# Kernel optimization log

Measured on AMD Instinct MI355X. Metric: run time of the kernel, lower is better.

## Reference

```python
import jax, jax.numpy as jnp
import numpy as np
from jax.scipy.special import gammaln, xlogy

DIM = 1536
HEADS = 8
DK = 64
DV = 64
BS = 128
N = 1536
NRPF = 192  # num_rel_pos_features, divisible by 6
B = 2


def _positional_embed(n, feat):
    # [2n-1, feat] relative positional basis (exponential, central-mask, gamma),
    # each duplicated with sign(d) asymmetric variant.
    f = feat // 6
    d = jnp.arange(-n + 1, n, dtype=jnp.float32)
    ad = jnp.abs(d)[:, None]  # [2n-1, 1]
    # exponential: log-spaced half lives
    half_life = 2.0 ** jnp.linspace(3.0, float(np.log2(n)), f)
    e_exp = jnp.exp(-float(np.log(2.0)) / half_life[None, :] * ad)
    # central mask: 1 if |d| < 2^i - 1
    widths = 2.0 ** jnp.arange(1, f + 1, dtype=jnp.float32) - 1.0
    e_cm = (widths[None, :] > ad).astype(jnp.float32)
    # gamma pdf, linearly spaced means
    std = n / (2.0 * f)
    mean = jnp.linspace(n / f, float(n), f)[None, :]
    conc = (mean / std) ** 2
    rate = mean / (std ** 2)
    log_unnorm = xlogy(conc - 1.0, ad) - rate * ad
    log_norm = gammaln(conc) - conc * jnp.log(rate)
    probs = jnp.exp(log_unnorm - log_norm) + 1e-8
    e_g = probs / jnp.max(probs, axis=-1, keepdims=True)
    emb = jnp.concatenate([e_exp, e_cm, e_g], axis=-1)  # [2n-1, 3f]
    return jnp.concatenate([emb, jnp.sign(d)[:, None] * emb], axis=-1)  # [2n-1, 6f]


def _relative_shift(t):
    # [B, H, N, 2N-1] -> [B, H, N, N] (Transformer-XL shift)
    b, h, t1, t2 = t.shape
    t = jnp.concatenate([jnp.zeros_like(t[..., :1]), t], axis=-1)  # [.., t2+1]
    t = t.reshape(b, h, t2 + 1, t1)[:, :, 1:, :].reshape(b, h, t1, t2)
    return t[..., :t1]


def setup_inputs() -> dict:
    key = jax.random.key(0)
    ks = jax.random.split(key, 10)
    x = jax.random.normal(ks[0], (B, N, DIM), dtype=jnp.float32)
    Wq = jax.random.normal(ks[1], (DIM, HEADS * DK), dtype=jnp.float32) * 0.02
    Wk = jax.random.normal(ks[2], (DIM, HEADS * DK), dtype=jnp.float32) * 0.02
    Wv = jax.random.normal(ks[3], (DIM, HEADS * DV), dtype=jnp.float32) * 0.02
    Wrel = jax.random.normal(ks[4], (NRPF, HEADS * DK), dtype=jnp.float32) * 0.02
    rel_content_bias = jax.random.normal(ks[5], (1, HEADS, 1, DK), dtype=jnp.float32)
    rel_pos_bias = jax.random.normal(ks[6], (1, HEADS, 1, DK), dtype=jnp.float32)
    # to_out is zero-init in the original; use small random so the output/grads are non-trivial
    Wo = jax.random.normal(ks[7], (HEADS * DV, DIM), dtype=jnp.float32) * 0.02
    bo = jnp.zeros((DIM,), dtype=jnp.float32)
    pos_embed = _positional_embed(N, NRPF)  # [2N-1, NRPF]
    # BigBird block-local window mask: blocks bi attend to blocks bi-1..bi+1
    bi = np.arange(N) // BS
    local_mask = jnp.asarray(np.abs(bi[:, None] - bi[None, :]) <= 1)  # [N, N] bool
    # a few global tokens per batch
    is_global = jnp.zeros((B, N), dtype=bool).at[:, :4].set(True)
    return {"x": x, "Wq": Wq, "Wk": Wk, "Wv": Wv, "Wrel": Wrel,
            "rel_content_bias": rel_content_bias, "rel_pos_bias": rel_pos_bias,
            "Wo": Wo, "bo": bo, "pos_embed": pos_embed,
            "local_mask": local_mask, "is_global": is_global}


def reference(x, Wq, Wk, Wv, Wrel, rel_content_bias, rel_pos_bias, Wo, bo,
              pos_embed, local_mask, is_global):
    b, n, _ = x.shape
    h, dk = rel_content_bias.shape[1], rel_content_bias.shape[-1]
    dv = Wv.shape[-1] // h
    scale = dk ** -0.5
    q = (x @ Wq).reshape(b, n, h, dk).transpose(0, 2, 1, 3) * scale  # [b,h,n,dk]
    k = (x @ Wk).reshape(b, n, h, dk).transpose(0, 2, 1, 3)
    v = (x @ Wv).reshape(b, n, h, dv).transpose(0, 2, 1, 3)
    content_logits = jnp.einsum('bhid,bhjd->bhij', q + rel_content_bias, k)
    rel_k = (pos_embed @ Wrel).reshape(2 * n - 1, h, dk).transpose(1, 0, 2)  # [h,2n-1,dk]
    rel_logits = jnp.einsum('bhid,hjd->bhij', q + rel_pos_bias, rel_k)  # [b,h,n,2n-1]
    logits = content_logits + _relative_shift(rel_logits)
    attn_bool = (local_mask[None, None] | is_global[:, None, :, None]
                 | is_global[:, None, None, :])
    logits = jnp.where(attn_bool, logits.astype(jnp.float32), -jnp.inf)
    attn = jax.nn.softmax(logits, axis=-1)
    out = jnp.einsum('bhij,bhjd->bhid', attn, v.astype(jnp.float32))
    out = out.astype(x.dtype).transpose(0, 2, 1, 3).reshape(b, n, h * dv)
    return out @ Wo + bo
```

## Files before the change

### kernel.cpp

```cpp
#include <hip/hip_runtime.h>
#include <math.h>

#define NSEQ 1536
#define HD3  1536
#define RKLD 512
#define RLEN 3071
#define NB   12

typedef __attribute__((ext_vector_type(8))) short bf16x8;
typedef __attribute__((ext_vector_type(4))) float f32x4;
typedef _Float16 f16x8 __attribute__((ext_vector_type(8)));
typedef _Float16 f16x4 __attribute__((ext_vector_type(4)));

__device__ __forceinline__ unsigned short f2bf(float f) {
    union { float f; unsigned u; } v; v.f = f;
    unsigned r = v.u + 0x7fffu + ((v.u >> 16) & 1u);
    return (unsigned short)(r >> 16);
}
__device__ __forceinline__ float bf2f(unsigned short s) {
    union { unsigned u; float f; } v; v.u = ((unsigned)s) << 16;
    return v.f;
}
__device__ __forceinline__ void cp16(const void* g, void* l) {
    __builtin_amdgcn_global_load_lds(
        (const __attribute__((address_space(1))) void*)g,
        (__attribute__((address_space(3))) void*)l, 16, 0, 0);
}

#define KSWZ(row, d) ((row) * 64 + (((((d) >> 3) ^ ((row) & 7))) << 3) + ((d) & 7))
#define PSWZ(r, j)   ((r) * 128 + (((((j) >> 3) ^ ((r) & 15))) << 3) + ((j) & 7))
#define VSTR 136

__global__ __launch_bounds__(256) void splitf16(
    const float* __restrict__ X, _Float16* __restrict__ H, int n4)
{
    int i = blockIdx.x * 256 + threadIdx.x;
    if (i >= n4) return;
    float4 v = ((const float4*)X)[i];
    union { _Float16 h[4]; ushort4 u; } c;
    c.h[0] = (_Float16)v.x; c.h[1] = (_Float16)v.y;
    c.h[2] = (_Float16)v.z; c.h[3] = (_Float16)v.w;
    ((ushort4*)H)[i] = c.u;
}

__device__ __forceinline__ void wsplit_body16(
    const float* __restrict__ W, _Float16* __restrict__ T,
    int K, int N, int n_off, int ldt, float scale, int bx, int by)
{
    __shared__ float tile[64][65];
    const int k0 = by * 64, n0 = bx * 64;
    const int t = threadIdx.x;
    const int rr = t >> 4, c4 = (t & 15) * 4;
#pragma unroll
    for (int p = 0; p < 4; ++p) {
        int r = p * 16 + rr;
        float4 v = *(const float4*)(W + (size_t)(k0 + r) * N + n0 + c4);
        tile[r][c4 + 0] = v.x; tile[r][c4 + 1] = v.y;
        tile[r][c4 + 2] = v.z; tile[r][c4 + 3] = v.w;
    }
    __syncthreads();
#pragma unroll
    for (int p = 0; p < 4; ++p) {
        int n = p * 16 + rr;
        union { _Float16 h[4]; ushort4 u; } cc;
        cc.h[0] = (_Float16)(tile[c4 + 0][n] * scale);
        cc.h[1] = (_Float16)(tile[c4 + 1][n] * scale);
        cc.h[2] = (_Float16)(tile[c4 + 2][n] * scale);
        cc.h[3] = (_Float16)(tile[c4 + 3][n] * scale);
        size_t o = (size_t)(n_off + n0 + n) * ldt + k0 + c4;
        *(ushort4*)(T + o) = cc.u;
    }
}

__global__ __launch_bounds__(256) void wsplit_qkv16(
    const float* __restrict__ Wq, const float* __restrict__ Wk,
    const float* __restrict__ Wv, _Float16* __restrict__ T)
{
    const int z = blockIdx.z;
    const float* W = (z == 0) ? Wq : (z == 1) ? Wk : Wv;
    wsplit_body16(W, T, 1536, 512, z * 512, 1536, (z == 0) ? 0.125f : 1.f,
                  blockIdx.x, blockIdx.y);
}

__global__ __launch_bounds__(256) void wsplit_t16(
    const float* __restrict__ W, _Float16* __restrict__ T,
    int K, int N, int n_off, int ldt, float scale)
{
    wsplit_body16(W, T, K, N, n_off, ldt, scale, blockIdx.x, blockIdx.y);
}

__global__ __launch_bounds__(256) void gemm_f16k(
    const _Float16* __restrict__ A,
    const _Float16* __restrict__ B,
    const float* __restrict__ bias, float* __restrict__ C,
    int M, int N, int K)
{
    __shared__ _Float16 sA[2][4096];
    __shared__ _Float16 sB[2][4096];
    const int t = threadIdx.x;
    const int wave = t >> 6, lane = t & 63;
    const int nwg = gridDim.x * gridDim.y;
    const int lin = blockIdx.y * gridDim.x + blockIdx.x;
    const int swz = (lin & 7) * (nwg >> 3) + (lin >> 3);
    const int bx = swz % gridDim.x, by = swz / gridDim.x;
    const int m0 = by * 64, n0 = bx * 64;
    const int wm = (wave >> 1) * 32, wn = (wave & 1) * 32;
    const int fr = lane & 15, quad = lane >> 4;

    f32x4 acc[2][2];
#pragma unroll
    for (int i = 0; i < 2; ++i)
#pragma unroll
        for (int j = 0; j < 2; ++j)
#pragma unroll
            for (int c = 0; c < 4; ++c) acc[i][j][c] = 0.f;

    const int nsteps = K >> 6;

#define STAGE(k0, buf)                                                        \
    {                                                                         \
        _Pragma("unroll")                                                     \
        for (int it = 0; it < 2; ++it) {                                      \
            int cidx = it * 256 + t;                                          \
            int row = cidx >> 3, slot = cidx & 7;                             \
            int gch = slot ^ (row & 7);                                       \
            size_t goA = (size_t)(m0 + row) * K + (k0) + gch * 8;             \
            size_t goB = (size_t)(n0 + row) * K + (k0) + gch * 8;             \
            cp16(A + goA, &sA[buf][it * 2048 + wave * 512]);                  \
            cp16(B + goB, &sB[buf][it * 2048 + wave * 512]);                  \
        }                                                                     \
    }

    STAGE(0, 0);
    for (int s = 0; s < nsteps; ++s) {
        const int buf = s & 1;
        __syncthreads();
        if (s + 1 < nsteps) STAGE((s + 1) * 64, buf ^ 1);

        f16x8 fa[2][2], fb[2][2];
#pragma unroll
        for (int ti = 0; ti < 2; ++ti)
#pragma unroll
            for (int kc = 0; kc < 2; ++kc) {
                fa[ti][kc] = *(const f16x8*)&sA[buf][KSWZ(wm + ti * 16 + fr,
                                                          kc * 32 + quad * 8)];
                fb[ti][kc] = *(const f16x8*)&sB[buf][KSWZ(wn + ti * 16 + fr,
                                                          kc * 32 + quad * 8)];
            }
#pragma unroll
        for (int ti = 0; ti < 2; ++ti)
#pragma unroll
            for (int tj = 0; tj < 2; ++tj)
#pragma unroll
                for (int kc = 0; kc < 2; ++kc)
                    acc[ti][tj] = __builtin_amdgcn_mfma_f32_16x16x32_f16(
                        fa[ti][kc], fb[tj][kc], acc[ti][tj], 0, 0, 0);
    }
#undef STAGE

#pragma unroll
    for (int ti = 0; ti < 2; ++ti) {
        int rowb = m0 + wm + ti * 16 + quad * 4;
#pragma unroll
        for (int tj = 0; tj < 2; ++tj) {
            int col = n0 + wn + tj * 16 + fr;
            float bb = bias ? bias[col] : 0.f;
#pragma unroll
            for (int j2 = 0; j2 < 4; ++j2)
                C[(size_t)(rowb + j2) * N + col] = acc[ti][tj][j2] + bb;
        }
    }
}

__global__ __launch_bounds__(256) void gemm_f32(
    const float* __restrict__ A, const float* __restrict__ B,
    const float* __restrict__ bias, float* __restrict__ C,
    int M, int N, int K, float alpha)
{
    __shared__ float As_[16][68];
    __shared__ float Bs_[16][68];
    const int t = threadIdx.x;
    const int m0 = blockIdx.y * 64;
    const int n0 = blockIdx.x * 64;
    const int tm = t >> 4, tn = t & 15;
    float acc[4][4];
#pragma unroll
    for (int i = 0; i < 4; ++i)
#pragma unroll
        for (int j = 0; j < 4; ++j) acc[i][j] = 0.f;

    for (int k0 = 0; k0 < K; k0 += 16) {
        {
            int row = t >> 2;
            int kk  = (t & 3) * 4;
            int gm  = m0 + row;
            float4 av = make_float4(0.f, 0.f, 0.f, 0.f);
            if (gm < M) av = *(const float4*)(A + (size_t)gm * K + k0 + kk);
            As_[kk + 0][row] = av.x; As_[kk + 1][row] = av.y;
            As_[kk + 2][row] = av.z; As_[kk + 3][row] = av.w;
        }
        {
            int kk = t >> 4;
            int nn = (t & 15) * 4;
            float4 bv = *(const float4*)(B + (size_t)(k0 + kk) * N + n0 + nn);
            *(float4*)&Bs_[kk][nn] = bv;
        }
        __syncthreads();
#pragma unroll
        for (int kk = 0; kk < 16; ++kk) {
            float a[4], bb[4];
            *(float4*)&a[0]  = *(const float4*)&As_[kk][tm * 4];
            *(float4*)&bb[0] = *(const float4*)&Bs_[kk][tn * 4];
#pragma unroll
            for (int i = 0; i < 4; ++i)
#pragma unroll
                for (int j = 0; j < 4; ++j)
                    acc[i][j] = fmaf(a[i], bb[j], acc[i][j]);
        }
        __syncthreads();
    }
#pragma unroll
    for (int i = 0; i < 4; ++i) {
        int gm = m0 + tm * 4 + i;
        if (gm < M) {
            float* crow = C + (size_t)gm * N + n0 + tn * 4;
#pragma unroll
            for (int j = 0; j < 4; ++j) {
                float vv = acc[i][j] * alpha;
                if (bias) vv += bias[n0 + tn * 4 + j];
                crow[j] = vv;
            }
        }
    }
}

__global__ __launch_bounds__(256) void drk_kernel(
    const float* __restrict__ rkk, const float* __restrict__ cb,
    const float* __restrict__ rb, float* __restrict__ drk)
{
    int idx = blockIdx.x * 256 + threadIdx.x;
    if (idx >= 8 * RLEN) return;
    int jj = idx >> 3, h = idx & 7;
    const float* rrow = rkk + (size_t)jj * RKLD + h * 64;
    float s0 = 0, s1 = 0, s2 = 0, s3 = 0;
#pragma unroll
    for (int d4 = 0; d4 < 16; ++d4) {
        float4 rv = *(const float4*)(rrow + d4 * 4);
        float dx = rb[h * 64 + d4 * 4 + 0] - cb[h * 64 + d4 * 4 + 0];
        float dy = rb[h * 64 + d4 * 4 + 1] - cb[h * 64 + d4 * 4 + 1];
        float dz = rb[h * 64 + d4 * 4 + 2] - cb[h * 64 + d4 * 4 + 2];
        float dw = rb[h * 64 + d4 * 4 + 3] - cb[h * 64 + d4 * 4 + 3];
        s0 = fmaf(dx, rv.x, s0); s1 = fmaf(dy, rv.y, s1);
        s2 = fmaf(dz, rv.z, s2); s3 = fmaf(dw, rv.w, s3);
    }
    drk[h * RLEN + jj] = (s0 + s1) + (s2 + s3);
}

__global__ __launch_bounds__(256) void relb_mfma(
    const float* __restrict__ qkv, const float* __restrict__ rkk,
    const float* __restrict__ rb, _Float16* __restrict__ relbT)
{
    __shared__ _Float16 sR[8192];
    const int ct = blockIdx.x, bi = blockIdx.y, bh = blockIdx.z;
    const int b = bh >> 3, h = bh & 7;
    const int i0 = bi * 128;
    const int c0 = (bi == 0) ? 0 : (bi - 1) * 128;
    const int jjbase = c0 - i0 - 127 + (NSEQ - 1) + ct * 128;
    const int t = threadIdx.x;
    const int wave = t >> 6, lane = t & 63;
    const int fr = lane & 15, quad = lane >> 4;

#pragma unroll
    for (int it = 0; it < 8; ++it) {
        int lin = it * 256 + t;
        int row = lin >> 4, d4 = (lin & 15) * 4;
        const float* rp = rkk + (size_t)(jjbase + row) * RKLD + h * 64 + d4;
        float4 v = *(const float4*)rp;
        union { _Float16 h[4]; ushort4 u; } cc;
        cc.h[0] = (_Float16)v.x; cc.h[1] = (_Float16)v.y;
        cc.h[2] = (_Float16)v.z; cc.h[3] = (_Float16)v.w;
        *(ushort4*)&sR[KSWZ(row, d4)] = cc.u;
    }
    f16x8 qf[2][2];
    {
        const float* Qg = qkv + ((size_t)(b * NSEQ + i0)) * HD3 + h * 64;
#pragma unroll
        for (int ti = 0; ti < 2; ++ti)
#pragma unroll
            for (int kc = 0; kc < 2; ++kc) {
                int m = wave * 32 + ti * 16 + fr;
                int k8 = kc * 32 + quad * 8;
                const float* qp = Qg + (size_t)m * HD3 + k8;
                const float* cp = rb + h * 64 + k8;
                float4 qa = *(const float4*)qp,  qb = *(const float4*)(qp + 4);
                float4 ca = *(const float4*)cp,  c2 = *(const float4*)(cp + 4);
                _Float16 hx[8] = {
                    (_Float16)(qa.x + ca.x), (_Float16)(qa.y + ca.y),
                    (_Float16)(qa.z + ca.z), (_Float16)(qa.w + ca.w),
                    (_Float16)(qb.x + c2.x), (_Float16)(qb.y + c2.y),
                    (_Float16)(qb.z + c2.z), (_Float16)(qb.w + c2.w)};
                qf[ti][kc] = *(f16x8*)hx;
            }
    }
    __syncthreads();

    f32x4 sacc[2][8];
#pragma unroll
    for (int i = 0; i < 2; ++i)
#pragma unroll
        for (int j = 0; j < 8; ++j)
#pragma unroll
            for (int c = 0; c < 4; ++c) sacc[i][j][c] = 0.f;

#pragma unroll
    for (int kc = 0; kc < 2; ++kc) {
        f16x8 bv[8];
#pragma unroll
        for (int tj = 0; tj < 8; ++tj)
            bv[tj] = *(const f16x8*)&sR[KSWZ(tj * 16 + fr, kc * 32 + quad * 8)];
#pragma unroll
        for (int ti = 0; ti < 2; ++ti)
#pragma unroll
            for (int tj = 0; tj < 8; ++tj)
                sacc[ti][tj] = __builtin_amdgcn_mfma_f32_16x16x32_f16(
                    qf[ti][kc], bv[tj], sacc[ti][tj], 0, 0, 0);
    }

    size_t bb_ = ((size_t)bh * NB + bi) * 512;
#pragma unroll
    for (int ti = 0; ti < 2; ++ti) {
        int mr = wave * 32 + ti * 16 + quad * 4;
#pragma unroll
        for (int tj = 0; tj < 8; ++tj) {
            int ccg = ct * 128 + tj * 16 + fr;
#pragma unroll
            for (int reg = 0; reg < 4; ++reg) {
                int r = mr + reg;
                int jl = ccg - 127 + r;
                if (jl >= 0)
                    relbT[(bb_ + jl) * 128 + r] = (_Float16)sacc[ti][tj][reg];
            }
        }
    }
}

__global__ __launch_bounds__(256) void attn_mfma(
    const float* __restrict__ qkv, const _Float16* __restrict__ relbT,
    const float* __restrict__ cb, float* __restrict__ O_part,
    float* __restrict__ l_part)
{
    __shared__ unsigned short sKP[16384];
    __shared__ unsigned short sVt[64 * VSTR];
    const int ct = blockIdx.x, bi = blockIdx.y, bh = blockIdx.z;
    const int b = bh >> 3, h = bh & 7;
    const int i0 = bi * 128;
    const int c0 = (bi == 0) ? 0 : (bi - 1) * 128;
    const int c1 = (bi == NB - 1) ? NSEQ : (bi + 2) * 128;
    const int ctile = c0 + ct * 128;
    const int t = threadIdx.x;
    const int wave = t >> 6, lane = t & 63;
    const int fr = lane & 15, quad = lane >> 4;

    float* Op = O_part + (((size_t)ct * 16 + bh) * NSEQ + i0) * 64;
    float* lp = l_part + ((size_t)ct * 16 + bh) * NSEQ + i0;

    if (ctile >= c1) {
        for (int k2 = t; k2 < 8192; k2 += 256) Op[k2] = 0.f;
        if (t < 128) lp[t] = 0.f;
        return;
    }

    {
        const float* Kg = qkv + ((size_t)(b * NSEQ + ctile)) * HD3 + 512 + h * 64;
#pragma unroll
        for (int it = 0; it < 8; ++it) {
            int lin = it * 256 + t;
            int row = lin >> 4, d4 = (lin & 15) * 4;
            float4 v = *(const float4*)(Kg + (size_t)row * HD3 + d4);
            union { _Float16 h[4]; ushort4 u; } cc;
            cc.h[0] = (_Float16)v.x; cc.h[1] = (_Float16)v.y;
            cc.h[2] = (_Float16)v.z; cc.h[3] = (_Float16)v.w;
            *(ushort4*)&sKP[KSWZ(row, d4)] = cc.u;
        }
    }
    {
        const float* Vg = qkv + ((size_t)(b * NSEQ + ctile)) * HD3 + 1024 + h * 64;
#pragma unroll
        for (int it = 0; it < 2; ++it) {
            int lin = it * 256 + t;
            int r4 = (lin >> 4) * 4, d4 = (lin & 15) * 4;
            float4 v0 = *(const float4*)(Vg + (size_t)(r4 + 0) * HD3 + d4);
            float4 v1 = *(const float4*)(Vg + (size_t)(r4 + 1) * HD3 + d4);
            float4 v2 = *(const float4*)(Vg + (size_t)(r4 + 2) * HD3 + d4);
            float4 v3 = *(const float4*)(Vg + (size_t)(r4 + 3) * HD3 + d4);
            const float* p0 = (const float*)&v0;
            const float* p1 = (const float*)&v1;
            const float* p2 = (const float*)&v2;
            const float* p3 = (const float*)&v3;
#pragma unroll
            for (int dd = 0; dd < 4; ++dd) {
                ushort4 hh;
                hh.x = f2bf(p0[dd]); hh.y = f2bf(p1[dd]);
                hh.z = f2bf(p2[dd]); hh.w = f2bf(p3[dd]);
                *(ushort4*)&sVt[(d4 + dd) * VSTR + r4] = hh;
            }
        }
    }
    f16x8 qf[2][2];
    {
        const float* Qg = qkv + ((size_t)(b * NSEQ + i0)) * HD3 + h * 64;
#pragma unroll
        for (int ti = 0; ti < 2; ++ti)
#pragma unroll
            for (int kc = 0; kc < 2; ++kc) {
                int m = wave * 32 + ti * 16 + fr;
                int k8 = kc * 32 + quad * 8;
                const float* qp = Qg + (size_t)m * HD3 + k8;
                const float* cp = cb + h * 64 + k8;
                float4 qa = *(const float4*)qp,  qb = *(const float4*)(qp + 4);
                float4 ca = *(const float4*)cp,  c2 = *(const float4*)(cp + 4);
                _Float16 hx[8] = {
                    (_Float16)(qa.x + ca.x), (_Float16)(qa.y + ca.y),
                    (_Float16)(qa.z + ca.z), (_Float16)(qa.w + ca.w),
                    (_Float16)(qb.x + c2.x), (_Float16)(qb.y + c2.y),
                    (_Float16)(qb.z + c2.z), (_Float16)(qb.w + c2.w)};
                qf[ti][kc] = *(f16x8*)hx;
            }
    }
    __syncthreads();

    f32x4 sacc[2][8];
#pragma unroll
    for (int i = 0; i < 2; ++i)
#pragma unroll
        for (int j = 0; j < 8; ++j)
#pragma unroll
            for (int c = 0; c < 4; ++c) sacc[i][j][c] = 0.f;

#pragma unroll
    for (int kc = 0; kc < 2; ++kc) {
        f16x8 bv[8];
#pragma unroll
        for (int tj = 0; tj < 8; ++tj)
            bv[tj] = *(const f16x8*)&sKP[KSWZ(tj * 16 + fr, kc * 32 + quad * 8)];
#pragma unroll
        for (int ti = 0; ti < 2; ++ti)
#pragma unroll
            for (int tj = 0; tj < 8; ++tj)
                sacc[ti][tj] = __builtin_amdgcn_mfma_f32_16x16x32_f16(
                    qf[ti][kc], bv[tj], sacc[ti][tj], 0, 0, 0);
    }
    __syncthreads();

    const _Float16* relbase = relbT + (((size_t)bh * NB + bi) * 512 + ct * 128) * 128;
    float lsum[2][4] = {{0.f, 0.f, 0.f, 0.f}, {0.f, 0.f, 0.f, 0.f}};
#pragma unroll
    for (int ti = 0; ti < 2; ++ti) {
        int mr = wave * 32 + ti * 16 + quad * 4;
#pragma unroll
        for (int tj = 0; tj < 8; ++tj) {
            int j = tj * 16 + fr;
            f16x4 rl = *(const f16x4*)&relbase[(size_t)j * 128 + mr];
#pragma unroll
            for (int reg = 0; reg < 4; ++reg) {
                int r = mr + reg;
                float p = __expf(sacc[ti][tj][reg] + (float)rl[reg]);
                unsigned short pb = f2bf(p);
                lsum[ti][reg] += bf2f(pb);
                sKP[PSWZ(r, j)] = pb;
            }
        }
    }
#pragma unroll
    for (int m2 = 1; m2 < 16; m2 <<= 1)
#pragma unroll
        for (int ti = 0; ti < 2; ++ti)
#pragma unroll
            for (int reg = 0; reg < 4; ++reg)
                lsum[ti][reg] += __shfl_xor(lsum[ti][reg], m2, 64);
    if (fr == 0) {
#pragma unroll
        for (int ti = 0; ti < 2; ++ti) {
            int mr = wave * 32 + ti * 16 + quad * 4;
#pragma unroll
            for (int reg = 0; reg < 4; ++reg)
                lp[mr + reg] = lsum[ti][reg];
        }
    }

    f32x4 oacc[4][2];
#pragma unroll
    for (int i = 0; i < 4; ++i)
#pragma unroll
        for (int j = 0; j < 2; ++j)
#pragma unroll
            for (int c = 0; c < 4; ++c) oacc[i][j][c] = 0.f;

#pragma unroll
    for (int kc = 0; kc < 4; ++kc) {
        bf16x8 pbv[2];
#pragma unroll
        for (int rt2 = 0; rt2 < 2; ++rt2) {
            int r = (wave * 2 + rt2) * 16 + fr;
            pbv[rt2] = *(const bf16x8*)&sKP[PSWZ(r, kc * 32 + quad * 8)];
        }
#pragma unroll
        for (int dt = 0; dt < 4; ++dt) {
            bf16x8 av = *(const bf16x8*)&sVt[(dt * 16 + fr) * VSTR + kc * 32 + quad * 8];
#pragma unroll
            for (int rt2 = 0; rt2 < 2; ++rt2)
                oacc[dt][rt2] = __builtin_amdgcn_mfma_f32_16x16x32_bf16(
                    av, pbv[rt2], oacc[dt][rt2], 0, 0, 0);
        }
    }
#pragma unroll
    for (int dt = 0; dt < 4; ++dt)
#pragma unroll
        for (int rt2 = 0; rt2 < 2; ++rt2) {
            int r = (wave * 2 + rt2) * 16 + fr;
            int d = dt * 16 + quad * 4;
            float4 ov = make_float4(oacc[dt][rt2][0], oacc[dt][rt2][1],
                                    oacc[dt][rt2][2], oacc[dt][rt2][3]);
            *(float4*)(Op + (size_t)r * 64 + d) = ov;
        }
}

__global__ __launch_bounds__(128) void attn_gcols(
    const float* __restrict__ qkv, const float* __restrict__ rkk,
    const float* __restrict__ drk, const float* __restrict__ cb,
    float* __restrict__ O_part, float* __restrict__ l_part)
{
    const int bi = blockIdx.x + 2, bh = blockIdx.y;
    const int b = bh >> 3, h = bh & 7;
    const int i = bi * 128 + threadIdx.x;
    float qc[64];
    {
        const float* qrow = qkv + (size_t)(b * NSEQ + i) * HD3 + h * 64;
#pragma unroll
        for (int d4 = 0; d4 < 16; ++d4) {
            float4 qv = *(const float4*)(qrow + d4 * 4);
            float4 cv = *(const float4*)(cb + h * 64 + d4 * 4);
            qc[4 * d4 + 0] = qv.x + cv.x;
            qc[4 * d4 + 1] = qv.y + cv.y;
            qc[4 * d4 + 2] = qv.z + cv.z;
            qc[4 * d4 + 3] = qv.w + cv.w;
        }
    }
    float O[64];
#pragma unroll
    for (int d = 0; d < 64; ++d) O[d] = 0.f;
    float l = 0.f;
    for (int j = 0; j < 4; ++j) {
        const float* krow = qkv + ((size_t)(b * NSEQ + j)) * HD3 + 512 + h * 64;
        int jj = j - i + (NSEQ - 1);
        const float* rrow = rkk + (size_t)jj * RKLD + h * 64;
        float s0 = 0, s1 = 0, s2 = 0, s3 = 0;
#pragma unroll
        for (int d4 = 0; d4 < 16; ++d4) {
            float4 kv = *(const float4*)(krow + d4 * 4);
            float4 rv = *(const float4*)(rrow + d4 * 4);
            s0 = fmaf(qc[4 * d4 + 0], kv.x + rv.x, s0);
            s1 = fmaf(qc[4 * d4 + 1], kv.y + rv.y, s1);
            s2 = fmaf(qc[4 * d4 + 2], kv.z + rv.z, s2);
            s3 = fmaf(qc[4 * d4 + 3], kv.w + rv.w, s3);
        }
        float p = __expf((s0 + s1) + (s2 + s3) + drk[h * RLEN + jj]);
        l += p;
        const float* vrow = krow + 512;
#pragma unroll
        for (int d4 = 0; d4 < 16; ++d4) {
            float4 vf = *(const float4*)(vrow + d4 * 4);
            O[4 * d4 + 0] = fmaf(p, vf.x, O[4 * d4 + 0]);
            O[4 * d4 + 1] = fmaf(p, vf.y, O[4 * d4 + 1]);
            O[4 * d4 + 2] = fmaf(p, vf.z, O[4 * d4 + 2]);
            O[4 * d4 + 3] = fmaf(p, vf.w, O[4 * d4 + 3]);
        }
    }
    float* Op = O_part + ((size_t)bh * NSEQ + i) * 64;
#pragma unroll
    for (int d4 = 0; d4 < 16; ++d4) {
        float4 cur = *(float4*)(Op + d4 * 4);
        cur.x += O[4 * d4 + 0]; cur.y += O[4 * d4 + 1];
        cur.z += O[4 * d4 + 2]; cur.w += O[4 * d4 + 3];
        *(float4*)(Op + d4 * 4) = cur;
    }
    l_part[(size_t)bh * NSEQ + i] += l;
}

__global__ __launch_bounds__(256) void grows_part(
    const float* __restrict__ qkv, const float* __restrict__ rkk,
    const float* __restrict__ drk, const float* __restrict__ cb,
    float* __restrict__ g_O, float* __restrict__ g_l)
{
    __shared__ float qc_s[64];
    __shared__ float p_s[128];
    __shared__ float obuf[4][64];
    __shared__ float lred[2];
    const int chunk = blockIdx.x;
    const int bhi = blockIdx.y;
    const int i = bhi & 3, h = (bhi >> 2) & 7, b = bhi >> 5;
    const int t = threadIdx.x;
    const int c0 = chunk * 128;
    if (t < 64)
        qc_s[t] = qkv[(size_t)(b * NSEQ + i) * HD3 + h * 64 + t] + cb[h * 64 + t];
    __syncthreads();
    if (t < 128) {
        int j = c0 + t;
        const float* krow = qkv + (size_t)(b * NSEQ + j) * HD3 + 512 + h * 64;
        int jj = j - i + (NSEQ - 1);
        const float* rrow = rkk + (size_t)jj * RKLD + h * 64;
        float s0 = 0, s1 = 0, s2 = 0, s3 = 0;
#pragma unroll
        for (int d4 = 0; d4 < 16; ++d4) {
            float4 kv = *(const float4*)(krow + d4 * 4);
            float4 rv = *(const float4*)(rrow + d4 * 4);
            float4 qv = *(const float4*)(&qc_s[d4 * 4]);
            s0 = fmaf(qv.x, kv.x + rv.x, s0);
            s1 = fmaf(qv.y, kv.y + rv.y, s1);
            s2 = fmaf(qv.z, kv.z + rv.z, s2);
            s3 = fmaf(qv.w, kv.w + rv.w, s3);
        }
        float p = __expf((s0 + s1) + (s2 + s3) + drk[h * RLEN + jj]);
        p_s[t] = p;
        float ls = p;
#pragma unroll
        for (int off = 32; off > 0; off >>= 1)
            ls += __shfl_down(ls, off, 64);
        if ((t & 63) == 0) lred[t >> 6] = ls;
    }
    __syncthreads();
    {
        const int d = t & 63, g = t >> 6;
        float a0 = 0, a1 = 0;
        const float* vbase = qkv + (size_t)(b * NSEQ + c0 + g * 32) * HD3 + 1024 + h * 64 + d;
#pragma unroll
        for (int j2 = 0; j2 < 32; j2 += 2) {
            a0 = fmaf(p_s[g * 32 + j2],     vbase[(size_t)j2 * HD3],       a0);
            a1 = fmaf(p_s[g * 32 + j2 + 1], vbase[(size_t)(j2 + 1) * HD3], a1);
        }
        obuf[g][d] = a0 + a1;
    }
    __syncthreads();
    if (t < 64) {
        float o = (obuf[0][t] + obuf[1][t]) + (obuf[2][t] + obuf[3][t]);
        g_O[((size_t)chunk * 64 + bhi) * 64 + t] = o;
        if (t == 0) g_l[chunk * 64 + bhi] = lred[0] + lred[1];
    }
}

__global__ __launch_bounds__(256) void norm_merge(
    const float* __restrict__ O_part, const float* __restrict__ l_part,
    const float* __restrict__ g_O, const float* __restrict__ g_l,
    _Float16* __restrict__ aoh)
{
    const int bh = blockIdx.y, b = bh >> 3, h = bh & 7;
    const int i = blockIdx.x * 16 + (threadIdx.x >> 4);
    const int d4 = threadIdx.x & 15;
    float ox = 0, oy = 0, oz = 0, ow = 0, l = 0;
    if (i < 4) {
        const int bhi = bh * 4 + i;
#pragma unroll
        for (int c = 0; c < 12; ++c) {
            const float* gp = g_O + ((size_t)c * 64 + bhi) * 64 + d4 * 4;
            ox += gp[0]; oy += gp[1]; oz += gp[2]; ow += gp[3];
            l += g_l[c * 64 + bhi];
        }
    } else {
#pragma unroll
        for (int s = 0; s < 3; ++s) {
            const float* Opp = O_part + (((size_t)s * 16 + bh) * NSEQ + i) * 64 + d4 * 4;
            float4 p = *(const float4*)Opp;
            ox += p.x; oy += p.y; oz += p.z; ow += p.w;
            l += l_part[((size_t)s * 16 + bh) * NSEQ + i];
        }
    }
    float inv = 1.f / l;
    union { _Float16 h[4]; ushort4 u; } cc;
    cc.h[0] = (_Float16)(ox * inv); cc.h[1] = (_Float16)(oy * inv);
    cc.h[2] = (_Float16)(oz * inv); cc.h[3] = (_Float16)(ow * inv);
    size_t o = ((size_t)(b * NSEQ + i)) * 512 + h * 64 + d4 * 4;
    *(ushort4*)(aoh + o) = cc.u;
}

extern "C" void kernel_launch(void* const* d_in, const int* in_sizes, int n_in,
                              void* d_out, int out_size, void* d_ws, size_t ws_size,
                              hipStream_t stream)
{
    const float* x    = (const float*)d_in[0];
    const float* Wq   = (const float*)d_in[1];
    const float* Wk   = (const float*)d_in[2];
    const float* Wv   = (const float*)d_in[3];
    const float* Wrel = (const float*)d_in[4];
    const float* cb   = (const float*)d_in[5];
    const float* rb   = (const float*)d_in[6];
    const float* Wo   = (const float*)d_in[7];
    const float* bo   = (const float*)d_in[8];
    const float* pe   = (const float*)d_in[9];
    float* out = (float*)d_out;

    float* ws = (float*)d_ws;
    float* qkv   = ws;
    float* rkbuf = ws + 4718592;
    float* drk   = ws + 6291456;
    _Float16* aoh = (_Float16*)(ws + 6316032);
    _Float16* woh = (_Float16*)(ws + 7888896);
    float* R = ws + 8675328;
    _Float16* relbT = (_Float16*)R;
    _Float16* xh  = (_Float16*)R;
    _Float16* wqh = (_Float16*)(R + 4718592);
    float* g_O = R + 6291456;
    float* g_l = R + 6340608;
    float* O_part = ws + 15753216;
    float* l_part = ws + 20471808;

    dim3 blk(256);
    splitf16<<<4608, blk, 0, stream>>>(x, xh, 1179648);
    wsplit_qkv16<<<dim3(8, 24, 3), blk, 0, stream>>>(Wq, Wk, Wv, wqh);
    wsplit_t16<<<dim3(24, 8), blk, 0, stream>>>(Wo, woh, 512, 1536, 0, 512, 1.f);
    gemm_f16k<<<dim3(24, 48), blk, 0, stream>>>(xh, wqh, nullptr, qkv,
                                                3072, 1536, 1536);
    gemm_f32<<<dim3(8, 48), blk, 0, stream>>>(pe, Wrel, nullptr, rkbuf, 3071, 512, 192, 1.f);
    drk_kernel<<<96, blk, 0, stream>>>(rkbuf, cb, rb, drk);
    relb_mfma<<<dim3(4, 12, 16), blk, 0, stream>>>(qkv, rkbuf, rb, relbT);
    attn_mfma<<<dim3(3, 12, 16), blk, 0, stream>>>(qkv, relbT, cb, O_part, l_part);
    attn_gcols<<<dim3(10, 16), dim3(128), 0, stream>>>(qkv, rkbuf, drk, cb, O_part, l_part);
    grows_part<<<dim3(12, 64), blk, 0, stream>>>(qkv, rkbuf, drk, cb, g_O, g_l);
    norm_merge<<<dim3(96, 16), blk, 0, stream>>>(O_part, l_part, g_O, g_l, aoh);
    gemm_f16k<<<dim3(24, 48), blk, 0, stream>>>(aoh, woh, bo, out,
                                                3072, 1536, 512);
}
```

Baseline: 268.2 us.

## Fuse weight splits, move rel-pos GEMM to f16 MFMA, fold global columns into attention

Three weight-transpose kernels (qkv, Wo, Wrel) are merged into one launch. The fp32 SIMT GEMM for pos_embed@Wrel is replaced by an f16 MFMA GEMM, with pos_embed converted to f16 first. The separate attn_gcols kernel is removed, and the first-4 global-column contributions are computed inside attn_mfma for the ct==0 tiles. This cuts launches and a read-modify-write pass over O_part, at the cost of f16 precision on rel-pos keys and extra work in some attention blocks. The rel-pos GEMM now runs with M=3072 over a 3071-row input, which relies on padding or workspace slack.

```diff
diff --git a/kernel.cpp b/kernel.cpp
--- a/kernel.cpp
+++ b/kernel.cpp
@@ -72,21 +72,24 @@
     }
 }
 
-__global__ __launch_bounds__(256) void wsplit_qkv16(
+__global__ __launch_bounds__(256) void wsplit_all(
     const float* __restrict__ Wq, const float* __restrict__ Wk,
-    const float* __restrict__ Wv, _Float16* __restrict__ T)
+    const float* __restrict__ Wv, const float* __restrict__ Wo,
+    const float* __restrict__ Wrel,
+    _Float16* __restrict__ Tqkv, _Float16* __restrict__ To,
+    _Float16* __restrict__ Trel)
 {
     const int z = blockIdx.z;
-    const float* W = (z == 0) ? Wq : (z == 1) ? Wk : Wv;
-    wsplit_body16(W, T, 1536, 512, z * 512, 1536, (z == 0) ? 0.125f : 1.f,
-                  blockIdx.x, blockIdx.y);
-}
-
-__global__ __launch_bounds__(256) void wsplit_t16(
-    const float* __restrict__ W, _Float16* __restrict__ T,
-    int K, int N, int n_off, int ldt, float scale)
-{
-    wsplit_body16(W, T, K, N, n_off, ldt, scale, blockIdx.x, blockIdx.y);
+    if (z < 3) {
+        const float* W = (z == 0) ? Wq : (z == 1) ? Wk : Wv;
+        wsplit_body16(W, Tqkv, 1536, 512, z * 512, 1536,
+                      (z == 0) ? 0.125f : 1.f, blockIdx.x, blockIdx.y);
+    } else if (z == 3) {
+        wsplit_body16(Wo, To, 512, 1536, 0, 512, 1.f, blockIdx.y, blockIdx.x);
+    } else {
+        if (blockIdx.y >= 3) return;
+        wsplit_body16(Wrel, Trel, 192, 512, 0, 192, 1.f, blockIdx.x, blockIdx.y);
+    }
 }
 
 __global__ __launch_bounds__(256) void gemm_f16k(
@@ -168,68 +171,6 @@
 #pragma unroll
             for (int j2 = 0; j2 < 4; ++j2)
                 C[(size_t)(rowb + j2) * N + col] = acc[ti][tj][j2] + bb;
-        }
-    }
-}
-
-__global__ __launch_bounds__(256) void gemm_f32(
-    const float* __restrict__ A, const float* __restrict__ B,
-    const float* __restrict__ bias, float* __restrict__ C,
-    int M, int N, int K, float alpha)
-{
-    __shared__ float As_[16][68];
-    __shared__ float Bs_[16][68];
-    const int t = threadIdx.x;
-    const int m0 = blockIdx.y * 64;
-    const int n0 = blockIdx.x * 64;
-    const int tm = t >> 4, tn = t & 15;
-    float acc[4][4];
-#pragma unroll
-    for (int i = 0; i < 4; ++i)
-#pragma unroll
-        for (int j = 0; j < 4; ++j) acc[i][j] = 0.f;
-
-    for (int k0 = 0; k0 < K; k0 += 16) {
-        {
-            int row = t >> 2;
-            int kk  = (t & 3) * 4;
-            int gm  = m0 + row;
-            float4 av = make_float4(0.f, 0.f, 0.f, 0.f);
-            if (gm < M) av = *(const float4*)(A + (size_t)gm * K + k0 + kk);
-            As_[kk + 0][row] = av.x; As_[kk + 1][row] = av.y;
-            As_[kk + 2][row] = av.z; As_[kk + 3][row] = av.w;
-        }
-        {
-            int kk = t >> 4;
-            int nn = (t & 15) * 4;
-            float4 bv = *(const float4*)(B + (size_t)(k0 + kk) * N + n0 + nn);
-            *(float4*)&Bs_[kk][nn] = bv;
-        }
-        __syncthreads();
-#pragma unroll
-        for (int kk = 0; kk < 16; ++kk) {
-            float a[4], bb[4];
-            *(float4*)&a[0]  = *(const float4*)&As_[kk][tm * 4];
-            *(float4*)&bb[0] = *(const float4*)&Bs_[kk][tn * 4];
-#pragma unroll
-            for (int i = 0; i < 4; ++i)
-#pragma unroll
-                for (int j = 0; j < 4; ++j)
-                    acc[i][j] = fmaf(a[i], bb[j], acc[i][j]);
-        }
-        __syncthreads();
-    }
-#pragma unroll
-    for (int i = 0; i < 4; ++i) {
-        int gm = m0 + tm * 4 + i;
-        if (gm < M) {
-            float* crow = C + (size_t)gm * N + n0 + tn * 4;
-#pragma unroll
-            for (int j = 0; j < 4; ++j) {
-                float vv = acc[i][j] * alpha;
-                if (bias) vv += bias[n0 + tn * 4 + j];
-                crow[j] = vv;
-            }
         }
     }
 }
@@ -346,11 +287,15 @@
 
 __global__ __launch_bounds__(256) void attn_mfma(
     const float* __restrict__ qkv, const _Float16* __restrict__ relbT,
+    const float* __restrict__ rkbuf, const float* __restrict__ drk,
     const float* __restrict__ cb, float* __restrict__ O_part,
     float* __restrict__ l_part)
 {
     __shared__ unsigned short sKP[16384];
     __shared__ unsigned short sVt[64 * VSTR];
+    __shared__ float p_g[128 * 4];
+    __shared__ __align__(16) float vg[4 * 64];
+    __shared__ float lg[128];
     const int ct = blockIdx.x, bi = blockIdx.y, bh = blockIdx.z;
     const int b = bh >> 3, h = bh & 7;
     const int i0 = bi * 128;
@@ -369,6 +314,8 @@
         if (t < 128) lp[t] = 0.f;
         return;
     }
+
+    const bool do_g = (ct == 0 && bi >= 2);
 
     {
         const float* Kg = qkv + ((size_t)(b * NSEQ + ctile)) * HD3 + 512 + h * 64;
@@ -403,6 +350,49 @@
                 hh.x = f2bf(p0[dd]); hh.y = f2bf(p1[dd]);
                 hh.z = f2bf(p2[dd]); hh.w = f2bf(p3[dd]);
                 *(ushort4*)&sVt[(d4 + dd) * VSTR + r4] = hh;
+            }
+        }
+    }
+    if (do_g) {
+        if (t < 128) {
+            const int r = t;
+            const int i = i0 + r;
+            const int jjb = NSEQ - 1 - i;
+            const float* qrow = qkv + (size_t)(b * NSEQ + i) * HD3 + h * 64;
+            const float* krow = qkv + (size_t)(b * NSEQ) * HD3 + 512 + h * 64;
+            const float* rrow = rkbuf + (size_t)jjb * RKLD + h * 64;
+            float s[4] = {0.f, 0.f, 0.f, 0.f};
+#pragma unroll
+            for (int d4 = 0; d4 < 16; ++d4) {
+                float4 qv = *(const float4*)(qrow + d4 * 4);
+                float4 cv = *(const float4*)(cb + h * 64 + d4 * 4);
+                float q0 = qv.x + cv.x, q1 = qv.y + cv.y;
+                float q2 = qv.z + cv.z, q3 = qv.w + cv.w;
+#pragma unroll
+                for (int j = 0; j < 4; ++j) {
+                    float4 kv = *(const float4*)(krow + (size_t)j * HD3 + d4 * 4);
+                    float4 rv = *(const float4*)(rrow + (size_t)j * RKLD + d4 * 4);
+                    s[j] = fmaf(q0, kv.x + rv.x, s[j]);
+                    s[j] = fmaf(q1, kv.y + rv.y, s[j]);
+                    s[j] = fmaf(q2, kv.z + rv.z, s[j]);
+                    s[j] = fmaf(q3, kv.w + rv.w, s[j]);
+                }
+            }
+            float l = 0.f;
+#pragma unroll
+            for (int j = 0; j < 4; ++j) {
+                float p = __expf(s[j] + drk[h * RLEN + jjb + j]);
+                p_g[r * 4 + j] = p;
+                l += p;
+            }
+            lg[r] = l;
+        } else {
+            int u = (t - 128) * 2;
+#pragma unroll
+            for (int w = 0; w < 2; ++w) {
+                int idx = u + w;
+                vg[idx] = qkv[(size_t)(b * NSEQ + (idx >> 6)) * HD3 + 1024
+                              + h * 64 + (idx & 63)];
             }
         }
     }
@@ -484,7 +474,7 @@
             int mr = wave * 32 + ti * 16 + quad * 4;
 #pragma unroll
             for (int reg = 0; reg < 4; ++reg)
-                lp[mr + reg] = lsum[ti][reg];
+                lp[mr + reg] = lsum[ti][reg] + (do_g ? lg[mr + reg] : 0.f);
         }
     }
 
@@ -514,77 +504,31 @@
         }
     }
 #pragma unroll
-    for (int dt = 0; dt < 4; ++dt)
-#pragma unroll
-        for (int rt2 = 0; rt2 < 2; ++rt2) {
-            int r = (wave * 2 + rt2) * 16 + fr;
+    for (int rt2 = 0; rt2 < 2; ++rt2) {
+        int r = (wave * 2 + rt2) * 16 + fr;
+        float pg0 = 0.f, pg1 = 0.f, pg2 = 0.f, pg3 = 0.f;
+        if (do_g) {
+            pg0 = p_g[r * 4 + 0]; pg1 = p_g[r * 4 + 1];
+            pg2 = p_g[r * 4 + 2]; pg3 = p_g[r * 4 + 3];
+        }
+#pragma unroll
+        for (int dt = 0; dt < 4; ++dt) {
             int d = dt * 16 + quad * 4;
             float4 ov = make_float4(oacc[dt][rt2][0], oacc[dt][rt2][1],
                                     oacc[dt][rt2][2], oacc[dt][rt2][3]);
+            if (do_g) {
+                float4 v0 = *(const float4*)&vg[0 * 64 + d];
+                float4 v1 = *(const float4*)&vg[1 * 64 + d];
+                float4 v2 = *(const float4*)&vg[2 * 64 + d];
+                float4 v3 = *(const float4*)&vg[3 * 64 + d];
+                ov.x += pg0 * v0.x + pg1 * v1.x + pg2 * v2.x + pg3 * v3.x;
+                ov.y += pg0 * v0.y + pg1 * v1.y + pg2 * v2.y + pg3 * v3.y;
+                ov.z += pg0 * v0.z + pg1 * v1.z + pg2 * v2.z + pg3 * v3.z;
+                ov.w += pg0 * v0.w + pg1 * v1.w + pg2 * v2.w + pg3 * v3.w;
+            }
             *(float4*)(Op + (size_t)r * 64 + d) = ov;
         }
-}
-
-__global__ __launch_bounds__(128) void attn_gcols(
-    const float* __restrict__ qkv, const float* __restrict__ rkk,
-    const float* __restrict__ drk, const float* __restrict__ cb,
-    float* __restrict__ O_part, float* __restrict__ l_part)
-{
-    const int bi = blockIdx.x + 2, bh = blockIdx.y;
-    const int b = bh >> 3, h = bh & 7;
-    const int i = bi * 128 + threadIdx.x;
-    float qc[64];
-    {
-        const float* qrow = qkv + (size_t)(b * NSEQ + i) * HD3 + h * 64;
-#pragma unroll
-        for (int d4 = 0; d4 < 16; ++d4) {
-            float4 qv = *(const float4*)(qrow + d4 * 4);
-            float4 cv = *(const float4*)(cb + h * 64 + d4 * 4);
-            qc[4 * d4 + 0] = qv.x + cv.x;
-            qc[4 * d4 + 1] = qv.y + cv.y;
-            qc[4 * d4 + 2] = qv.z + cv.z;
-            qc[4 * d4 + 3] = qv.w + cv.w;
-        }
-    }
-    float O[64];
-#pragma unroll
-    for (int d = 0; d < 64; ++d) O[d] = 0.f;
-    float l = 0.f;
-    for (int j = 0; j < 4; ++j) {
-        const float* krow = qkv + ((size_t)(b * NSEQ + j)) * HD3 + 512 + h * 64;
-        int jj = j - i + (NSEQ - 1);
-        const float* rrow = rkk + (size_t)jj * RKLD + h * 64;
-        float s0 = 0, s1 = 0, s2 = 0, s3 = 0;
-#pragma unroll
-        for (int d4 = 0; d4 < 16; ++d4) {
-            float4 kv = *(const float4*)(krow + d4 * 4);
-            float4 rv = *(const float4*)(rrow + d4 * 4);
-            s0 = fmaf(qc[4 * d4 + 0], kv.x + rv.x, s0);
-            s1 = fmaf(qc[4 * d4 + 1], kv.y + rv.y, s1);
-            s2 = fmaf(qc[4 * d4 + 2], kv.z + rv.z, s2);
-            s3 = fmaf(qc[4 * d4 + 3], kv.w + rv.w, s3);
-        }
-        float p = __expf((s0 + s1) + (s2 + s3) + drk[h * RLEN + jj]);
-        l += p;
-        const float* vrow = krow + 512;
-#pragma unroll
-        for (int d4 = 0; d4 < 16; ++d4) {
-            float4 vf = *(const float4*)(vrow + d4 * 4);
-            O[4 * d4 + 0] = fmaf(p, vf.x, O[4 * d4 + 0]);
-            O[4 * d4 + 1] = fmaf(p, vf.y, O[4 * d4 + 1]);
-            O[4 * d4 + 2] = fmaf(p, vf.z, O[4 * d4 + 2]);
-            O[4 * d4 + 3] = fmaf(p, vf.w, O[4 * d4 + 3]);
-        }
-    }
-    float* Op = O_part + ((size_t)bh * NSEQ + i) * 64;
-#pragma unroll
-    for (int d4 = 0; d4 < 16; ++d4) {
-        float4 cur = *(float4*)(Op + d4 * 4);
-        cur.x += O[4 * d4 + 0]; cur.y += O[4 * d4 + 1];
-        cur.z += O[4 * d4 + 2]; cur.w += O[4 * d4 + 3];
-        *(float4*)(Op + d4 * 4) = cur;
-    }
-    l_part[(size_t)bh * NSEQ + i] += l;
+    }
 }
 
 __global__ __launch_bounds__(256) void grows_part(
@@ -712,18 +656,22 @@
     float* g_l = R + 6340608;
     float* O_part = ws + 15753216;
     float* l_part = ws + 20471808;
+    _Float16* peh   = (_Float16*)(ws + 20545536);
+    _Float16* wrelT = (_Float16*)(ws + 20840448);
 
     dim3 blk(256);
     splitf16<<<4608, blk, 0, stream>>>(x, xh, 1179648);
-    wsplit_qkv16<<<dim3(8, 24, 3), blk, 0, stream>>>(Wq, Wk, Wv, wqh);
-    wsplit_t16<<<dim3(24, 8), blk, 0, stream>>>(Wo, woh, 512, 1536, 0, 512, 1.f);
+    splitf16<<<576, blk, 0, stream>>>(pe, peh, 147408);
+    wsplit_all<<<dim3(8, 24, 5), blk, 0, stream>>>(Wq, Wk, Wv, Wo, Wrel,
+                                                   wqh, woh, wrelT);
     gemm_f16k<<<dim3(24, 48), blk, 0, stream>>>(xh, wqh, nullptr, qkv,
                                                 3072, 1536, 1536);
-    gemm_f32<<<dim3(8, 48), blk, 0, stream>>>(pe, Wrel, nullptr, rkbuf, 3071, 512, 192, 1.f);
+    gemm_f16k<<<dim3(8, 48), blk, 0, stream>>>(peh, wrelT, nullptr, rkbuf,
+                                               3072, 512, 192);
     drk_kernel<<<96, blk, 0, stream>>>(rkbuf, cb, rb, drk);
     relb_mfma<<<dim3(4, 12, 16), blk, 0, stream>>>(qkv, rkbuf, rb, relbT);
-    attn_mfma<<<dim3(3, 12, 16), blk, 0, stream>>>(qkv, relbT, cb, O_part, l_part);
-    attn_gcols<<<dim3(10, 16), dim3(128), 0, stream>>>(qkv, rkbuf, drk, cb, O_part, l_part);
+    attn_mfma<<<dim3(3, 12, 16), blk, 0, stream>>>(qkv, relbT, rkbuf, drk, cb,
+                                                   O_part, l_part);
     grows_part<<<dim3(12, 64), blk, 0, stream>>>(qkv, rkbuf, drk, cb, g_O, g_l);
     norm_merge<<<dim3(96, 16), blk, 0, stream>>>(O_part, l_part, g_O, g_l, aoh);
     gemm_f16k<<<dim3(24, 48), blk, 0, stream>>>(aoh, woh, bo, out,
```

New measurement: 242.8 us. -9.5%, faster.
